# Optimization experiments

Hardware: AMD Instinct MI355X
Metric: run time of the kernel (lower is better)

Reference implementation:

```python
import jax, jax.numpy as jnp
import numpy as np

BETA = 0.25


def setup_inputs() -> dict:
    key = jax.random.key(0)
    k1, k2 = jax.random.split(key)
    z = jax.random.normal(k1, (8, 256, 16, 16, 16), dtype=jnp.float32)
    n_codes, dim = 2048, 256
    # original init: uniform(-1/n_codes, 1/n_codes)
    emb = jax.random.uniform(k2, (n_codes, dim), dtype=jnp.float32,
                             minval=-1.0 / n_codes, maxval=1.0 / n_codes)
    return {"z": z, "emb": emb}


def reference(z, emb):
    B, C, D, H, W = z.shape  # C == embedding_dim
    # channels-last flatten: [B*D*H*W, C]
    z_flat = jnp.transpose(z, (0, 2, 3, 4, 1)).reshape(-1, C)
    # squared L2 distances to each code: [N, K]
    dist = (jnp.sum(z_flat * z_flat, axis=1, keepdims=True)
            + jnp.sum(emb * emb, axis=1)
            - 2.0 * jnp.dot(z_flat, emb.T))
    idx = jnp.argmin(dist, axis=1)  # [N] int
    # FAITHFUL to original: gathered codes are reshaped directly to z.shape
    # (B, C, D, H, W) WITHOUT undoing the channels-last permute.
    z_q = jnp.take(emb, idx, axis=0).reshape(z.shape)
    commitment_loss = jnp.mean((jax.lax.stop_gradient(z_q) - z) ** 2)
    codebook_loss = jnp.mean((z_q - jax.lax.stop_gradient(z)) ** 2)
    vq_loss = codebook_loss + BETA * commitment_loss
    z_q_st = z + jax.lax.stop_gradient(z_q - z)  # straight-through
    return (z_q_st, vq_loss, idx)
```

## Files before the change

kernel.cpp:

```cpp
#include <hip/hip_runtime.h>
#include <float.h>

#define N_PTS    32768
#define N_CODES  2048
#define DIM      256
#define S_STRIDE 4096
#define B_STRIDE 1048576
#define N_ELEM   8388608

#define MARGIN   8e-4f

#define WS_PARTIAL 0
#define WS_E2      512
#define WS_EB      8704
#define WS_ZT      1057280
#define WS_TMIN    17834496
#define WS_EMBP    WS_ZT

typedef unsigned short ushort_t;
typedef short bf16x8 __attribute__((ext_vector_type(8)));
typedef float f32x4 __attribute__((ext_vector_type(4)));

__device__ __forceinline__ ushort_t f2bf(float v) {
    const unsigned u = __float_as_uint(v);
    return (ushort_t)((u + 0x7FFFu + ((u >> 16) & 1u)) >> 16);
}

__device__ __forceinline__ void async_copy16(void* lds, const void* g) {
    __builtin_amdgcn_global_load_lds(
        (const __attribute__((address_space(1))) unsigned int*)g,
        (__attribute__((address_space(3))) unsigned int*)lds, 16, 0, 0);
}

__device__ __forceinline__ void nt_store4(float* p, f32x4 v) {
    __builtin_nontemporal_store(v, reinterpret_cast<f32x4*>(p));
}

__global__ void conv_emb_kernel(const float* __restrict__ emb, ushort_t* __restrict__ eb) {
    const int gid = blockIdx.x * 256 + threadIdx.x;
    const int k = gid >> 6, c4 = gid & 63;
    const float4 u = *reinterpret_cast<const float4*>(emb + (size_t)k * DIM + c4 * 4);
    ushort4 v; v.x = f2bf(u.x); v.y = f2bf(u.y); v.z = f2bf(u.z); v.w = f2bf(u.w);
    *reinterpret_cast<ushort4*>(eb + (size_t)k * DIM + c4 * 4) = v;
}

__global__ void perm_emb_kernel(const float* __restrict__ emb, float* __restrict__ embp) {
    const int gid = blockIdx.x * 256 + threadIdx.x;
    const int ql = gid & 15, c4 = (gid >> 4) & 63, g = gid >> 10;
    const float4 u = reinterpret_cast<const float4*>(emb)[(size_t)(g * 16 + ql) * 64 + c4];
    reinterpret_cast<float4*>(embp)[gid] = u;
}

__global__ void e2p_kernel(const float* __restrict__ emb, float* __restrict__ e2,
                           float* __restrict__ partial) {
    const int k = blockIdx.x * 256 + threadIdx.x;
    if (blockIdx.x == 0 && threadIdx.x < 64) partial[threadIdx.x] = 0.f;
    const float* base = emb + (size_t)k * DIM;
    float half[2];
    #pragma unroll
    for (int h = 0; h < 2; ++h) {
        float r[8];
        #pragma unroll
        for (int j = 0; j < 8; ++j) { const float v = base[h * 128 + j]; r[j] = __fmul_rn(v, v); }
        for (int t = 8; t < 128; t += 8)
            #pragma unroll
            for (int j = 0; j < 8; ++j) {
                const float v = base[h * 128 + t + j];
                r[j] = __fadd_rn(r[j], __fmul_rn(v, v));
            }
        half[h] = __fadd_rn(__fadd_rn(__fadd_rn(r[0], r[1]), __fadd_rn(r[2], r[3])),
                            __fadd_rn(__fadd_rn(r[4], r[5]), __fadd_rn(r[6], r[7])));
    }
    e2[k] = __fadd_rn(half[0], half[1]);
}

__global__ void transpose_kernel(const float* __restrict__ z, ushort_t* __restrict__ zt) {
    __shared__ ushort_t lt[64][72];
    const int bx = blockIdx.x;
    const int b = bx >> 8, cg = (bx >> 6) & 3, sg = bx & 63;
    const int c0 = cg * 64, s0 = sg * 64;
    const int t = threadIdx.x;
    {
        const int cl = t >> 4, s4 = t & 15;
        #pragma unroll
        for (int j = 0; j < 4; ++j) {
            const int c = cl + 16 * j;
            const float4 u = *reinterpret_cast<const float4*>(
                z + (size_t)b * B_STRIDE + (size_t)(c0 + c) * S_STRIDE + s0 + s4 * 4);
            ushort4 v; v.x = f2bf(u.x); v.y = f2bf(u.y); v.z = f2bf(u.z); v.w = f2bf(u.w);
            *reinterpret_cast<ushort4*>(&lt[c][s4 * 4]) = v;
        }
    }
    __syncthreads();
    {
        const int sl = t >> 4, c4 = t & 15;
        #pragma unroll
        for (int j = 0; j < 4; ++j) {
            const int s = sl + 16 * j;
            ushort4 v;
            v.x = lt[c4 * 4 + 0][s]; v.y = lt[c4 * 4 + 1][s];
            v.z = lt[c4 * 4 + 2][s]; v.w = lt[c4 * 4 + 3][s];
            *reinterpret_cast<ushort4*>(zt + (size_t)(b * 4096 + s0 + s) * DIM + c0 + c4 * 4) = v;
        }
    }
}

__global__ __launch_bounds__(256, 2) void screen_kernel(
    const ushort_t* __restrict__ zt, const ushort_t* __restrict__ eb,
    const float* __restrict__ e2, float* __restrict__ tmin)
{
    __shared__ char lds[49152];
    __shared__ float e2s[256];
    const int tid = threadIdx.x;
    const int x = blockIdx.x;
    const int bm = (x & 7) * 32 + ((x >> 3) & 31), bn = x >> 8;
    const int n0 = bm * 128, k0 = bn * 256;
    e2s[tid] = e2[k0 + tid];
    const int wv = tid >> 6, lane = tid & 63;
    const int col = lane & 15, quad = lane >> 4;
    const int cswz = col & 7;

    f32x4 acc[8][4];
    #pragma unroll
    for (int i = 0; i < 8; ++i)
        #pragma unroll
        for (int j = 0; j < 4; ++j) acc[i][j] = (f32x4){0.f, 0.f, 0.f, 0.f};

    for (int kc = 0; kc < 4; ++kc) {
        __syncthreads();
        #pragma unroll
        for (int it = 0; it < 12; ++it) {
            const int L = tid + it * 256;
            if (L < 1024) {
                const int row = L >> 3, pc = L & 7, c = pc ^ (row & 7);
                async_copy16(lds + L * 16,
                             zt + ((size_t)(n0 + row) * DIM + kc * 64 + c * 8));
            } else {
                const int L2 = L - 1024;
                const int row = L2 >> 3, pc = L2 & 7, c = pc ^ (row & 7);
                async_copy16(lds + 16384 + L2 * 16,
                             eb + ((size_t)(k0 + row) * DIM + kc * 64 + c * 8));
            }
        }
        __syncthreads();
        #pragma unroll
        for (int s = 0; s < 2; ++s) {
            const int pc = (s * 4 + quad) ^ cswz;
            bf16x8 bq[4];
            #pragma unroll
            for (int j = 0; j < 4; ++j) {
                const int brow = wv * 64 + j * 16 + col;
                bq[j] = *reinterpret_cast<const bf16x8*>(lds + 16384 + (brow * 8 + pc) * 16);
            }
            #pragma unroll
            for (int i = 0; i < 8; ++i) {
                const int arow = i * 16 + col;
                const bf16x8 af = *reinterpret_cast<const bf16x8*>(lds + (arow * 8 + pc) * 16);
                #pragma unroll
                for (int j = 0; j < 4; ++j)
                    acc[i][j] = __builtin_amdgcn_mfma_f32_16x16x32_bf16(af, bq[j], acc[i][j], 0, 0, 0);
            }
        }
    }
    #pragma unroll
    for (int i = 0; i < 8; ++i) {
        #pragma unroll
        for (int j = 0; j < 4; ++j) {
            const float e2v = e2s[wv * 64 + j * 16 + col];
            float tm[4];
            #pragma unroll
            for (int r = 0; r < 4; ++r) tm[r] = fmaf(-2.f, acc[i][j][r], e2v);
            #pragma unroll
            for (int off = 1; off < 16; off <<= 1)
                #pragma unroll
                for (int r = 0; r < 4; ++r) tm[r] = fminf(tm[r], __shfl_xor(tm[r], off));
            if (col == 0) {
                const int g = bn * 16 + wv * 4 + j;
                const int nb = n0 + i * 16 + quad * 4;
                #pragma unroll
                for (int r = 0; r < 4; ++r) tmin[(size_t)(nb + r) * 128 + g] = tm[r];
            }
        }
    }
}

__global__ __launch_bounds__(256, 3) void exact_kernel(
    const float* __restrict__ z, const float* __restrict__ emb,
    const float* __restrict__ embp,
    const float* __restrict__ e2, const float* __restrict__ tmin,
    float* __restrict__ outf, float* __restrict__ out_idx, float* __restrict__ partial)
{
    __shared__ float zs[32 * 260];
    const int tid = threadIdx.x;
    const int n0 = blockIdx.x * 32;
    const int b = n0 >> 12, s0 = n0 & 4095;
    {
        const int tq = tid & 7, cg = tid >> 3;
        for (int c = cg; c < DIM; c += 32) {
            const float4 u = *reinterpret_cast<const float4*>(
                z + (size_t)b * B_STRIDE + (size_t)c * S_STRIDE + s0 + tq * 4);
            zs[(tq * 4 + 0) * 260 + c] = u.x;
            zs[(tq * 4 + 1) * 260 + c] = u.y;
            zs[(tq * 4 + 2) * 260 + c] = u.z;
            zs[(tq * 4 + 3) * 260 + c] = u.w;
        }
    }
    __syncthreads();
    const int wv = tid >> 6, lane = tid & 63;
    const int quad = lane >> 4, ql = lane & 15;
    float lossacc = 0.f;

    float a[2][8];
    #pragma unroll
    for (int t = 0; t < 2; ++t) {
        const int n = n0 + wv * 8 + t * 4 + quad;
        #pragma unroll
        for (int i = 0; i < 8; ++i)
            a[t][i] = __builtin_nontemporal_load(tmin + (size_t)n * 128 + i * 16 + ql);
    }

    #pragma unroll
    for (int t = 0; t < 2; ++t) {
        const int p = wv * 8 + t * 4 + quad;
        const int n = n0 + p;
        const float* zr = &zs[p * 260];
        const int h = ql >> 3, j = ql & 7;
        float v0 = zr[h * 128 + j];
        float r = __fmul_rn(v0, v0);
        #pragma unroll
        for (int t2 = 1; t2 < 16; ++t2) {
            const float v = zr[h * 128 + j + 8 * t2];
            r = __fadd_rn(r, __fmul_rn(v, v));
        }
        { float v = __shfl_xor(r, 1); r = __fadd_rn(r, v); }
        { float v = __shfl_xor(r, 2); r = __fadd_rn(r, v); }
        { float v = __shfl_xor(r, 4); r = __fadd_rn(r, v); }
        const float z2n = __fadd_rn(__shfl(r, quad * 16), __shfl(r, quad * 16 + 8));
        float mn = fminf(fminf(fminf(a[t][0], a[t][1]), fminf(a[t][2], a[t][3])),
                         fminf(fminf(a[t][4], a[t][5]), fminf(a[t][6], a[t][7])));
        #pragma unroll
        for (int off = 1; off < 16; off <<= 1) mn = fminf(mn, __shfl_xor(mn, off));
        const float thr = mn + MARGIN;
        unsigned long long M0 = 0ull, M1 = 0ull;
        #pragma unroll
        for (int i = 0; i < 8; ++i) {
            const unsigned long long bal = __ballot(a[t][i] <= thr);
            const unsigned long long bits = (bal >> (quad * 16)) & 0xFFFFull;
            if (i < 4) M0 |= bits << (i * 16);
            else       M1 |= bits << ((i - 4) * 16);
        }
        float bs = FLT_MAX; int bk = 0x7FFFFFFF;
        while (__any((M0 | M1) != 0ull)) {
            int myt = -1;
            if (M0) { myt = __ffsll(M0) - 1; M0 &= M0 - 1; }
            else if (M1) { myt = 64 + __ffsll(M1) - 1; M1 &= M1 - 1; }
            if (myt >= 0) {
                const int kg = myt * 16 + ql;
                const float e2k = e2[kg];
                const float4* gp = reinterpret_cast<const float4*>(embp)
                                   + (size_t)myt * 1024 + ql;
                float4 pre[8];
                #pragma unroll
                for (int s8 = 0; s8 < 8; ++s8) pre[s8] = gp[s8 * 16];
                float dot = 0.f;
                #pragma unroll
                for (int seg = 0; seg < 8; ++seg) {
                    float4 cur[8];
                    #pragma unroll
                    for (int s8 = 0; s8 < 8; ++s8) cur[s8] = pre[s8];
                    if (seg < 7) {
                        #pragma unroll
                        for (int s8 = 0; s8 < 8; ++s8)
                            pre[s8] = gp[(seg + 1) * 128 + s8 * 16];
                    }
                    #pragma unroll
                    for (int s8 = 0; s8 < 8; ++s8) {
                        const int c4 = seg * 8 + s8;
                        const float4 zv = *reinterpret_cast<const float4*>(zr + c4 * 4);
                        dot = fmaf(zv.x, cur[s8].x, dot);
                        dot = fmaf(zv.y, cur[s8].y, dot);
                        dot = fmaf(zv.z, cur[s8].z, dot);
                        dot = fmaf(zv.w, cur[s8].w, dot);
                    }
                }
                const float A = __fadd_rn(z2n, e2k);
                const float s = __fsub_rn(A, __fmul_rn(2.f, dot));
                if (s < bs || (s == bs && kg < bk)) { bs = s; bk = kg; }
            }
        }
        #pragma unroll
        for (int off = 1; off < 16; off <<= 1) {
            const float os = __shfl_xor(bs, off);
            const int ok = __shfl_xor(bk, off);
            if (os < bs || (os == bs && ok < bk)) { bs = os; bk = ok; }
        }
        const float* eq = emb + (size_t)bk * DIM;
        float* op = outf + (size_t)n * DIM;
        #pragma unroll
        for (int jj = 0; jj < 4; ++jj) {
            const int c = (jj * 16 + ql) * 4;
            const float4 q4 = *reinterpret_cast<const float4*>(eq + c);
            f32x4 q; q[0] = q4.x; q[1] = q4.y; q[2] = q4.z; q[3] = q4.w;
            nt_store4(op + c, q);
            float d;
            d = q4.x - zr[c + 0]; lossacc = fmaf(d, d, lossacc);
            d = q4.y - zr[c + 1]; lossacc = fmaf(d, d, lossacc);
            d = q4.z - zr[c + 2]; lossacc = fmaf(d, d, lossacc);
            d = q4.w - zr[c + 3]; lossacc = fmaf(d, d, lossacc);
        }
        if (ql == 0) out_idx[n] = (float)bk;
    }
    #pragma unroll
    for (int off = 1; off < 64; off <<= 1) lossacc += __shfl_xor(lossacc, off);
    if (lane == 0) atomicAdd(&partial[blockIdx.x & 63], lossacc);
}

__global__ void finalize_kernel(const float* __restrict__ partial, float* __restrict__ out_loss) {
    float v = partial[threadIdx.x];
    #pragma unroll
    for (int off = 1; off < 64; off <<= 1) v += __shfl_xor(v, off);
    if (threadIdx.x == 0)
        *out_loss = v * 1.25f / (float)N_ELEM;
}

extern "C" void kernel_launch(void* const* d_in, const int* in_sizes, int n_in,
                              void* d_out, int out_size, void* d_ws, size_t ws_size,
                              hipStream_t stream) {
    const float* z = (const float*)d_in[0];
    const float* emb = (const float*)d_in[1];
    char* ws = (char*)d_ws;
    float* partial = (float*)(ws + WS_PARTIAL);
    float* e2 = (float*)(ws + WS_E2);
    ushort_t* eb = (ushort_t*)(ws + WS_EB);
    ushort_t* zt = (ushort_t*)(ws + WS_ZT);
    float* embp = (float*)(ws + WS_EMBP);
    float* tmin = (float*)(ws + WS_TMIN);
    float* outf = (float*)d_out;
    float* out_loss = outf + N_ELEM;
    float* out_idx = outf + N_ELEM + 1;

    conv_emb_kernel<<<512, 256, 0, stream>>>(emb, eb);
    e2p_kernel<<<N_CODES / 256, 256, 0, stream>>>(emb, e2, partial);
    transpose_kernel<<<2048, 256, 0, stream>>>(z, zt);
    screen_kernel<<<2048, 256, 0, stream>>>(zt, eb, e2, tmin);
    perm_emb_kernel<<<512, 256, 0, stream>>>(emb, embp);
    exact_kernel<<<N_PTS / 32, 256, 0, stream>>>(z, emb, embp, e2, tmin, outf, out_idx, partial);
    finalize_kernel<<<1, 64, 0, stream>>>(partial, out_loss);
}
```

Baseline: 236.2 us.

## Double-buffer screen kernel LDS tiles with smaller K-chunks to overlap loads and MFMA

The distance screening GEMM now splits K into eight 32-wide chunks and keeps two LDS buffers. It issues async global-to-LDS copies for the next chunk while MFMAs run on the current one, and the LDS swizzle is adjusted to match the 4-column row layout. The aim is to hide global-load latency that the old load-sync-compute loop left exposed. In exchange there are more barrier rounds and less work per chunk, while LDS size stays the same.

```diff
diff --git a/kernel.cpp b/kernel.cpp
--- a/kernel.cpp
+++ b/kernel.cpp
@@ -118,7 +118,7 @@
     e2s[tid] = e2[k0 + tid];
     const int wv = tid >> 6, lane = tid & 63;
     const int col = lane & 15, quad = lane >> 4;
-    const int cswz = col & 7;
+    const int pcr = quad ^ ((col >> 1) & 3);
 
     f32x4 acc[8][4];
     #pragma unroll
@@ -126,42 +126,53 @@
         #pragma unroll
         for (int j = 0; j < 4; ++j) acc[i][j] = (f32x4){0.f, 0.f, 0.f, 0.f};
 
-    for (int kc = 0; kc < 4; ++kc) {
-        __syncthreads();
-        #pragma unroll
-        for (int it = 0; it < 12; ++it) {
-            const int L = tid + it * 256;
-            if (L < 1024) {
-                const int row = L >> 3, pc = L & 7, c = pc ^ (row & 7);
-                async_copy16(lds + L * 16,
-                             zt + ((size_t)(n0 + row) * DIM + kc * 64 + c * 8));
-            } else {
-                const int L2 = L - 1024;
-                const int row = L2 >> 3, pc = L2 & 7, c = pc ^ (row & 7);
-                async_copy16(lds + 16384 + L2 * 16,
-                             eb + ((size_t)(k0 + row) * DIM + kc * 64 + c * 8));
-            }
-        }
-        __syncthreads();
-        #pragma unroll
-        for (int s = 0; s < 2; ++s) {
-            const int pc = (s * 4 + quad) ^ cswz;
+    #define STAGE(kc_, half_)                                                       \
+        {                                                                           \
+            const int base_ = (half_) * 24576;                                      \
+            _Pragma("unroll")                                                       \
+            for (int it = 0; it < 6; ++it) {                                        \
+                const int L = tid + it * 256;                                       \
+                if (L < 512) {                                                      \
+                    const int row = L >> 2, pc = L & 3, c = pc ^ ((row >> 1) & 3);  \
+                    async_copy16(lds + base_ + L * 16,                              \
+                                 zt + ((size_t)(n0 + row) * DIM + (kc_) * 32 + c * 8)); \
+                } else {                                                            \
+                    const int L2 = L - 512;                                         \
+                    const int row = L2 >> 2, pc = L2 & 3, c = pc ^ ((row >> 1) & 3);\
+                    async_copy16(lds + base_ + 8192 + L2 * 16,                      \
+                                 eb + ((size_t)(k0 + row) * DIM + (kc_) * 32 + c * 8)); \
+                }                                                                   \
+            }                                                                       \
+        }
+
+    STAGE(0, 0);
+    __syncthreads();
+    #pragma unroll
+    for (int kc = 0; kc < 8; ++kc) {
+        const int cur = kc & 1;
+        if (kc < 7) STAGE(kc + 1, cur ^ 1);
+        {
+            const char* ab = lds + cur * 24576;
+            const char* bb = ab + 8192;
             bf16x8 bq[4];
             #pragma unroll
             for (int j = 0; j < 4; ++j) {
                 const int brow = wv * 64 + j * 16 + col;
-                bq[j] = *reinterpret_cast<const bf16x8*>(lds + 16384 + (brow * 8 + pc) * 16);
+                bq[j] = *reinterpret_cast<const bf16x8*>(bb + (brow * 4 + pcr) * 16);
             }
             #pragma unroll
             for (int i = 0; i < 8; ++i) {
                 const int arow = i * 16 + col;
-                const bf16x8 af = *reinterpret_cast<const bf16x8*>(lds + (arow * 8 + pc) * 16);
+                const bf16x8 af = *reinterpret_cast<const bf16x8*>(ab + (arow * 4 + pcr) * 16);
                 #pragma unroll
                 for (int j = 0; j < 4; ++j)
                     acc[i][j] = __builtin_amdgcn_mfma_f32_16x16x32_bf16(af, bq[j], acc[i][j], 0, 0, 0);
             }
         }
-    }
+        __syncthreads();
+    }
+    #undef STAGE
+
     #pragma unroll
     for (int i = 0; i < 8; ++i) {
         #pragma unroll
```

New measurement: 258.8 us. 9.6% more time.
